# Kernel optimization log

Hardware: AMD Instinct MI355X
Metric: run time of the kernel (lower is better)

## Reference

```python
import jax, jax.numpy as jnp
import numpy as np

N = 50000      # nodes
E = 800000     # edges (avg degree 16)
IN = 256       # in_features
F1 = 32        # gnn_features per head
F2 = 32        # out_features per head
H = 8          # heads
NEG_SLOPE = 0.2


def setup_inputs() -> dict:
    key = jax.random.key(0)
    ks = jax.random.split(key, 12)
    s = 0.05
    return {
        "x":   jax.random.normal(ks[0], (N, IN), jnp.float32),
        "W1":  jax.random.normal(ks[1], (IN, H * F1), jnp.float32) * s,
        "al1": jax.random.normal(ks[2], (H, F1), jnp.float32) * s,
        "ar1": jax.random.normal(ks[3], (H, F1), jnp.float32) * s,
        "b1":  jnp.zeros((H, F1), jnp.float32),
        "W2":  jax.random.normal(ks[4], (F1, H * F2), jnp.float32) * s,
        "al2": jax.random.normal(ks[5], (H, F2), jnp.float32) * s,
        "ar2": jax.random.normal(ks[6], (H, F2), jnp.float32) * s,
        "b2":  jnp.zeros((H, F2), jnp.float32),
        "src": jax.random.randint(ks[7], (E,), 0, N, jnp.int32),
        "dst": jax.random.randint(ks[8], (E,), 0, N, jnp.int32),
    }


def _gat_layer(x, W, al, ar, b, src, dst):
    """One DGL-style GATConv. x:[N,Fin] -> [N,H,F]."""
    n, h, f = x.shape[0], al.shape[0], al.shape[1]
    z = (x @ W).reshape(n, h, f)                      # [N,H,F] projected feats
    el = jnp.einsum('nhf,hf->nh', z, al)              # src attention logits
    er = jnp.einsum('nhf,hf->nh', z, ar)              # dst attention logits
    e = el[src] + er[dst]                             # [E,H]
    e = jnp.where(e >= 0, e, NEG_SLOPE * e)           # LeakyReLU(0.2)
    # segmented (per-destination) softmax over incoming edges
    m = jax.ops.segment_max(e, dst, num_segments=n)   # [N,H]
    ex = jnp.exp(e - m[dst])                          # [E,H]
    denom = jax.ops.segment_sum(ex, dst, num_segments=n)
    alpha = ex / denom[dst]                           # [E,H]
    # weighted scatter-aggregate
    out = jax.ops.segment_sum(alpha[:, :, None] * z[src], dst, num_segments=n)
    return out + b[None]                              # [N,H,F]


def reference(x, W1, al1, ar1, b1, W2, al2, ar2, b2, src, dst):
    h = _gat_layer(x, W1, al1, ar1, b1, src, dst).mean(axis=1)   # [N,F1]
    h = jax.nn.elu(h)                                            # Dropout(0.5) = identity in eval
    out = _gat_layer(h, W2, al2, ar2, b2, src, dst).mean(axis=1) # [N,F2]
    return out
```

## Files before the change

### kernel.cpp

```cpp
#include <hip/hip_runtime.h>
#include <hip/hip_fp16.h>
#include <math.h>

#define IN_F 256
#define NHEAD 8
#define FDIM 32
#define SCAN_B 512

__device__ inline unsigned pkh2(float x, float y) {
  __half2 h = __floats2half2_rn(x, y);
  return *reinterpret_cast<unsigned*>(&h);
}


__global__ __launch_bounds__(256) void hist_k(const int* __restrict__ dst,
                                              int* __restrict__ deg, int E) {
  int i = blockIdx.x * 256 + threadIdx.x;
  if (i < E) atomicAdd(&deg[dst[i]], 1);
}

__global__ __launch_bounds__(SCAN_B) void scan1_k(const int* __restrict__ deg,
                                                  int* __restrict__ offs,
                                                  int* __restrict__ bsum, int N) {
  __shared__ int s[SCAN_B];
  int t = threadIdx.x;
  int i = blockIdx.x * SCAN_B + t;
  s[t] = (i < N) ? deg[i] : 0;
  __syncthreads();
  for (int off = 1; off < SCAN_B; off <<= 1) {
    int add = (t >= off) ? s[t - off] : 0;
    __syncthreads();
    s[t] += add;
    __syncthreads();
  }
  if (i < N) offs[i + 1] = s[t];
  if (t == SCAN_B - 1) bsum[blockIdx.x] = s[t];
}

__global__ __launch_bounds__(SCAN_B) void scan2_k(int* __restrict__ bsum, int nb) {
  __shared__ int s[SCAN_B];
  int t = threadIdx.x;
  s[t] = (t < nb) ? bsum[t] : 0;
  __syncthreads();
  for (int off = 1; off < SCAN_B; off <<= 1) {
    int add = (t >= off) ? s[t - off] : 0;
    __syncthreads();
    s[t] += add;
    __syncthreads();
  }
  if (t < nb) bsum[t] = (t == 0) ? 0 : s[t - 1];
}

__global__ __launch_bounds__(SCAN_B) void scan3_k(int* __restrict__ offs,
                                                  const int* __restrict__ bsum, int N) {
  int i = blockIdx.x * SCAN_B + threadIdx.x;
  if (i < N) offs[i + 1] += bsum[blockIdx.x];
  if (i == 0) offs[0] = 0;
}

__global__ __launch_bounds__(256) void scatter_k(const int* __restrict__ src,
                                                 const int* __restrict__ dst,
                                                 const int* __restrict__ offs,
                                                 int* __restrict__ cursor,
                                                 int* __restrict__ esrc, int E) {
  int i = blockIdx.x * 256 + threadIdx.x;
  if (i < E) {
    int d = dst[i];
    int pos = offs[d] + atomicAdd(&cursor[d], 1);
    esrc[pos] = src[i];
  }
}

__global__ __launch_bounds__(256) void gemm_xw_k(const float* __restrict__ A,
                                                 const float* __restrict__ B,
                                                 __half* __restrict__ Zh, int M) {
  __shared__ float AsF[16 * 196];
  __shared__ float BsF[16 * 196];
  int t = threadIdx.x;
  int tx = t & 15, ty = t >> 4;
  int row0 = blockIdx.x * 128, col0 = blockIdx.y * 128;
  float acc[8][8] = {};
  for (int kt = 0; kt < 256; kt += 16) {
#pragma unroll
    for (int i = 0; i < 2; ++i) {
      int idx = t + i * 256;
      int row = idx >> 2, q = idx & 3;
      float4 va = make_float4(0.f, 0.f, 0.f, 0.f);
      if (row0 + row < M)
        va = *reinterpret_cast<const float4*>(&A[(size_t)(row0 + row) * 256 + kt + q * 4]);
      int abase = (row >> 3) * 12 + (row & 7);
      AsF[(q * 4 + 0) * 196 + abase] = va.x;
      AsF[(q * 4 + 1) * 196 + abase] = va.y;
      AsF[(q * 4 + 2) * 196 + abase] = va.z;
      AsF[(q * 4 + 3) * 196 + abase] = va.w;
      int brow = idx >> 5, bc = idx & 31;
      float4 vb = *reinterpret_cast<const float4*>(&B[(size_t)(kt + brow) * 256 + col0 + bc * 4]);
      *reinterpret_cast<float4*>(&BsF[brow * 196 + (bc >> 1) * 12 + (bc & 1) * 4]) = vb;
    }
    __syncthreads();
#pragma unroll
    for (int kk = 0; kk < 16; ++kk) {
      float a[8], b[8];
      *reinterpret_cast<float4*>(&a[0]) = *reinterpret_cast<const float4*>(&AsF[kk * 196 + ty * 12]);
      *reinterpret_cast<float4*>(&a[4]) = *reinterpret_cast<const float4*>(&AsF[kk * 196 + ty * 12 + 4]);
      *reinterpret_cast<float4*>(&b[0]) = *reinterpret_cast<const float4*>(&BsF[kk * 196 + tx * 12]);
      *reinterpret_cast<float4*>(&b[4]) = *reinterpret_cast<const float4*>(&BsF[kk * 196 + tx * 12 + 4]);
#pragma unroll
      for (int i = 0; i < 8; ++i)
#pragma unroll
        for (int j = 0; j < 8; ++j) acc[i][j] = fmaf(a[i], b[j], acc[i][j]);
    }
    __syncthreads();
  }
#pragma unroll
  for (int i = 0; i < 8; ++i) {
    int r = row0 + ty * 8 + i;
    if (r < M) {
      uint4 w;
      w.x = pkh2(acc[i][0], acc[i][1]);
      w.y = pkh2(acc[i][2], acc[i][3]);
      w.z = pkh2(acc[i][4], acc[i][5]);
      w.w = pkh2(acc[i][6], acc[i][7]);
      *reinterpret_cast<uint4*>(&Zh[(size_t)r * 256 + col0 + tx * 8]) = w;
    }
  }
}

__global__ __launch_bounds__(256) void gemm_h_k(const float* __restrict__ Hmat,
                                                const float* __restrict__ W2,
                                                __half* __restrict__ Zh, int M) {
  __shared__ float Ws[32][256];
  __shared__ float Hs[32][20];
  int t = threadIdx.x;
  for (int i = t; i < 32 * 256; i += 256) Ws[i >> 8][i & 255] = W2[i];
  int row0 = blockIdx.x * 16;
  for (int i = t; i < 16 * 32; i += 256) {
    int r = i >> 5, k = i & 31;
    Hs[k][r] = (row0 + r < M) ? Hmat[(size_t)(row0 + r) * 32 + k] : 0.f;
  }
  __syncthreads();
  int tx = t & 63, ty = t >> 6;
  float acc[4][4] = {};
#pragma unroll
  for (int k = 0; k < 32; ++k) {
    float4 a4 = *reinterpret_cast<const float4*>(&Hs[k][ty * 4]);
    float4 b4 = *reinterpret_cast<const float4*>(&Ws[k][tx * 4]);
    float a[4] = {a4.x, a4.y, a4.z, a4.w};
    float b[4] = {b4.x, b4.y, b4.z, b4.w};
#pragma unroll
    for (int i = 0; i < 4; ++i)
#pragma unroll
      for (int j = 0; j < 4; ++j) acc[i][j] = fmaf(a[i], b[j], acc[i][j]);
  }
#pragma unroll
  for (int i = 0; i < 4; ++i) {
    int r = row0 + ty * 4 + i;
    if (r < M) {
      uint2 w;
      w.x = pkh2(acc[i][0], acc[i][1]);
      w.y = pkh2(acc[i][2], acc[i][3]);
      *reinterpret_cast<uint2*>(&Zh[(size_t)r * 256 + tx * 4]) = w;
    }
  }
}

__global__ __launch_bounds__(256) void logits_k(const __half* __restrict__ Zh,
                                                const float* __restrict__ al,
                                                const float* __restrict__ ar,
                                                float* __restrict__ el,
                                                float* __restrict__ er, int N) {
  int wave = threadIdx.x >> 6;
  int lane = threadIdx.x & 63;
  int n = blockIdx.x * 4 + wave;
  if (n >= N) return;
  uint2 u = *reinterpret_cast<const uint2*>(&Zh[(size_t)n * 256 + lane * 4]);
  float2 f0 = __half22float2(*reinterpret_cast<__half2*>(&u.x));
  float2 f1 = __half22float2(*reinterpret_cast<__half2*>(&u.y));
  float4 a4 = reinterpret_cast<const float4*>(al)[lane];
  float4 r4 = reinterpret_cast<const float4*>(ar)[lane];
  float pl = f0.x * a4.x + f0.y * a4.y + f1.x * a4.z + f1.y * a4.w;
  float pr = f0.x * r4.x + f0.y * r4.y + f1.x * r4.z + f1.y * r4.w;
  pl += __shfl_xor(pl, 1); pl += __shfl_xor(pl, 2); pl += __shfl_xor(pl, 4);
  pr += __shfl_xor(pr, 1); pr += __shfl_xor(pr, 2); pr += __shfl_xor(pr, 4);
  if ((lane & 7) == 0) {
    int h = lane >> 3;
    el[(size_t)n * 8 + h] = pl;
    er[(size_t)n * 8 + h] = pr;
  }
}

__global__ __launch_bounds__(256) void alpha_k(const float* __restrict__ el,
                                               const float* __restrict__ er,
                                               const int* __restrict__ offs,
                                               const int* __restrict__ esrc,
                                               float* __restrict__ alf,
                                               float* __restrict__ rden, int N) {
  int g = blockIdx.x * 256 + threadIdx.x;
  if (g >= N * NHEAD) return;
  int n = g >> 3, h = g & 7;
  int beg = offs[n], end = offs[n + 1];
  float er_h = er[g];
  float m = -INFINITY;
  for (int i = beg; i < end; ++i) {
    float e = el[(size_t)esrc[i] * 8 + h] + er_h;
    e = (e >= 0.f) ? e : 0.2f * e;
    m = fmaxf(m, e);
  }
  float s = 0.f;
  for (int i = beg; i < end; ++i) {
    float e = el[(size_t)esrc[i] * 8 + h] + er_h;
    e = (e >= 0.f) ? e : 0.2f * e;
    float ex = __expf(e - m);
    alf[(size_t)i * 8 + h] = ex;
    s += ex;
  }
  rden[g] = (end > beg) ? 1.f / s : 0.f;
}

template <bool LAYER1>
__global__ __launch_bounds__(256) void agg_k(const __half* __restrict__ Zh,
                                             const float* __restrict__ alf,
                                             const float* __restrict__ rden,
                                             const float* __restrict__ bias,
                                             const int* __restrict__ offs,
                                             const int* __restrict__ esrc,
                                             float* __restrict__ out, int N) {
  int wid = threadIdx.x >> 6, lane = threadIdx.x & 63;
  int n = blockIdx.x * 4 + wid;
  if (n >= N) return;
  int h = lane >> 3, q = lane & 7;
  int beg = offs[n], end = offs[n + 1];
  float4 acc = make_float4(0.f, 0.f, 0.f, 0.f);
#pragma unroll 4
  for (int i = beg; i < end; ++i) {
    int sidx = esrc[i];
    float a = alf[(size_t)i * 8 + h];
    uint2 u = *reinterpret_cast<const uint2*>(&Zh[(size_t)sidx * 256 + h * 32 + q * 4]);
    float2 f0 = __half22float2(*reinterpret_cast<__half2*>(&u.x));
    float2 f1 = __half22float2(*reinterpret_cast<__half2*>(&u.y));
    acc.x = fmaf(a, f0.x, acc.x);
    acc.y = fmaf(a, f0.y, acc.y);
    acc.z = fmaf(a, f1.x, acc.z);
    acc.w = fmaf(a, f1.y, acc.w);
  }
  float r = rden[(size_t)n * 8 + h];
  float4 b4 = *reinterpret_cast<const float4*>(&bias[h * 32 + q * 4]);
  float4 v;
  v.x = fmaf(acc.x, r, b4.x);
  v.y = fmaf(acc.y, r, b4.y);
  v.z = fmaf(acc.z, r, b4.z);
  v.w = fmaf(acc.w, r, b4.w);
#pragma unroll
  for (int off = 8; off < 64; off <<= 1) {
    v.x += __shfl_xor(v.x, off);
    v.y += __shfl_xor(v.y, off);
    v.z += __shfl_xor(v.z, off);
    v.w += __shfl_xor(v.w, off);
  }
  if (h == 0) {
    v.x *= 0.125f; v.y *= 0.125f; v.z *= 0.125f; v.w *= 0.125f;
    if (LAYER1) {
      v.x = (v.x > 0.f) ? v.x : expm1f(v.x);
      v.y = (v.y > 0.f) ? v.y : expm1f(v.y);
      v.z = (v.z > 0.f) ? v.z : expm1f(v.z);
      v.w = (v.w > 0.f) ? v.w : expm1f(v.w);
    }
    *reinterpret_cast<float4*>(&out[(size_t)n * 32 + q * 4]) = v;
  }
}


extern "C" void kernel_launch(void* const* d_in, const int* in_sizes, int n_in,
                              void* d_out, int out_size, void* d_ws, size_t ws_size,
                              hipStream_t stream) {
  const float* x   = (const float*)d_in[0];
  const float* W1  = (const float*)d_in[1];
  const float* al1 = (const float*)d_in[2];
  const float* ar1 = (const float*)d_in[3];
  const float* b1  = (const float*)d_in[4];
  const float* W2  = (const float*)d_in[5];
  const float* al2 = (const float*)d_in[6];
  const float* ar2 = (const float*)d_in[7];
  const float* b2  = (const float*)d_in[8];
  const int* src   = (const int*)d_in[9];
  const int* dst   = (const int*)d_in[10];
  float* out = (float*)d_out;

  const int N = in_sizes[0] / IN_F;
  const int E = in_sizes[9];

  char* p = (char*)d_ws;
  auto alloc = [&](size_t bytes) {
    char* q = p;
    p += (bytes + 255) & ~(size_t)255;
    return q;
  };
  __half* zh  = (__half*)alloc((size_t)N * 256 * 2);
  float* el   = (float*)alloc((size_t)N * 8 * 4);
  float* er   = (float*)alloc((size_t)N * 8 * 4);
  float* h1   = (float*)alloc((size_t)N * 32 * 4);
  float* alf  = (float*)alloc((size_t)E * 8 * 4);
  float* rden = (float*)alloc((size_t)N * 8 * 4);
  int* offs   = (int*)alloc((size_t)(N + 1) * 4);
  int* deg    = (int*)alloc((size_t)N * 4);
  int* cursor = (int*)alloc((size_t)N * 4);
  int* bsum   = (int*)alloc((size_t)SCAN_B * 4);
  int* esrc   = (int*)alloc((size_t)E * 4);

  hipMemsetAsync(deg, 0, (size_t)N * 4, stream);
  hipMemsetAsync(cursor, 0, (size_t)N * 4, stream);

  int nb = (N + SCAN_B - 1) / SCAN_B;
  hist_k<<<(E + 255) / 256, 256, 0, stream>>>(dst, deg, E);
  scan1_k<<<nb, SCAN_B, 0, stream>>>(deg, offs, bsum, N);
  scan2_k<<<1, SCAN_B, 0, stream>>>(bsum, nb);
  scan3_k<<<nb, SCAN_B, 0, stream>>>(offs, bsum, N);
  scatter_k<<<(E + 255) / 256, 256, 0, stream>>>(src, dst, offs, cursor, esrc, E);

  int nh_blocks = (N * NHEAD + 255) / 256;

  dim3 g1((N + 127) / 128, 2);
  gemm_xw_k<<<g1, 256, 0, stream>>>(x, W1, zh, N);
  logits_k<<<(N + 3) / 4, 256, 0, stream>>>(zh, al1, ar1, el, er, N);
  alpha_k<<<nh_blocks, 256, 0, stream>>>(el, er, offs, esrc, alf, rden, N);
  agg_k<true><<<(N + 3) / 4, 256, 0, stream>>>(zh, alf, rden, b1, offs, esrc, h1, N);

  gemm_h_k<<<(N + 15) / 16, 256, 0, stream>>>(h1, W2, zh, N);
  logits_k<<<(N + 3) / 4, 256, 0, stream>>>(zh, al2, ar2, el, er, N);
  alpha_k<<<nh_blocks, 256, 0, stream>>>(el, er, offs, esrc, alf, rden, N);
  agg_k<false><<<(N + 3) / 4, 256, 0, stream>>>(zh, alf, rden, b2, offs, esrc, out, N);
}
```

Before: 513.5 us.

## Replace FP32 SIMT projection GEMM with FP16 MFMA kernel using pre-transposed W1

The first-layer projection x@W1 now runs on MFMA 16x16x32 f16 instructions instead of a shared-memory tiled FP32 FMA GEMM. A small new kernel converts W1 to half and transposes it. The GEMM keeps each wave's A fragment in registers, converted from fp32 on load, and streams B straight from global memory (L2-resident) with no LDS staging. The trade-off is lower-precision inputs (fp16 x and W1), scalar 2-byte output stores, and one extra kernel launch.

After: 483.0 us. 6.0% less time.

```diff
diff --git a/kernel.cpp b/kernel.cpp
--- a/kernel.cpp
+++ b/kernel.cpp
@@ -6,6 +6,9 @@
 #define NHEAD 8
 #define FDIM 32
 #define SCAN_B 512
+
+typedef _Float16 f16x8 __attribute__((ext_vector_type(8)));
+typedef float f32x4 __attribute__((ext_vector_type(4)));
 
 __device__ inline unsigned pkh2(float x, float y) {
   __half2 h = __floats2half2_rn(x, y);
@@ -71,57 +74,55 @@
   }
 }
 
-__global__ __launch_bounds__(256) void gemm_xw_k(const float* __restrict__ A,
-                                                 const float* __restrict__ B,
-                                                 __half* __restrict__ Zh, int M) {
-  __shared__ float AsF[16 * 196];
-  __shared__ float BsF[16 * 196];
+__global__ __launch_bounds__(256) void w1cvt_k(const float* __restrict__ W1,
+                                               __half* __restrict__ W1t) {
+  __shared__ float s[16][17];
+  int bx = blockIdx.x * 16, by = blockIdx.y * 16;
+  int tx = threadIdx.x, ty = threadIdx.y;
+  s[ty][tx] = W1[(by + ty) * 256 + bx + tx];
+  __syncthreads();
+  W1t[(size_t)(bx + ty) * 256 + by + tx] = __float2half(s[tx][ty]);
+}
+
+__global__ __launch_bounds__(256) void gemm_xw_mfma_k(const float* __restrict__ X,
+                                                      const __half* __restrict__ W1t,
+                                                      __half* __restrict__ Zh, int M) {
   int t = threadIdx.x;
-  int tx = t & 15, ty = t >> 4;
-  int row0 = blockIdx.x * 128, col0 = blockIdx.y * 128;
-  float acc[8][8] = {};
-  for (int kt = 0; kt < 256; kt += 16) {
-#pragma unroll
-    for (int i = 0; i < 2; ++i) {
-      int idx = t + i * 256;
-      int row = idx >> 2, q = idx & 3;
-      float4 va = make_float4(0.f, 0.f, 0.f, 0.f);
-      if (row0 + row < M)
-        va = *reinterpret_cast<const float4*>(&A[(size_t)(row0 + row) * 256 + kt + q * 4]);
-      int abase = (row >> 3) * 12 + (row & 7);
-      AsF[(q * 4 + 0) * 196 + abase] = va.x;
-      AsF[(q * 4 + 1) * 196 + abase] = va.y;
-      AsF[(q * 4 + 2) * 196 + abase] = va.z;
-      AsF[(q * 4 + 3) * 196 + abase] = va.w;
-      int brow = idx >> 5, bc = idx & 31;
-      float4 vb = *reinterpret_cast<const float4*>(&B[(size_t)(kt + brow) * 256 + col0 + bc * 4]);
-      *reinterpret_cast<float4*>(&BsF[brow * 196 + (bc >> 1) * 12 + (bc & 1) * 4]) = vb;
+  int wv = t >> 6, l = t & 63;
+  int r = l & 15, kg = l >> 4;
+  int row0 = blockIdx.x * 64 + wv * 16;
+  int row = row0 + r;
+  int rowc = (row < M) ? row : (M - 1);
+
+  f16x8 a[8];
+  const float* xp = X + (size_t)rowc * 256 + kg * 8;
+#pragma unroll
+  for (int ks = 0; ks < 8; ++ks) {
+    float4 f0 = *reinterpret_cast<const float4*>(xp + ks * 32);
+    float4 f1 = *reinterpret_cast<const float4*>(xp + ks * 32 + 4);
+    f16x8 av;
+    av[0] = (_Float16)f0.x; av[1] = (_Float16)f0.y;
+    av[2] = (_Float16)f0.z; av[3] = (_Float16)f0.w;
+    av[4] = (_Float16)f1.x; av[5] = (_Float16)f1.y;
+    av[6] = (_Float16)f1.z; av[7] = (_Float16)f1.w;
+    a[ks] = av;
+  }
+
+#pragma unroll 4
+  for (int nf = 0; nf < 16; ++nf) {
+    int col = nf * 16 + r;
+    const f16x8* bp = reinterpret_cast<const f16x8*>(W1t + (size_t)col * 256 + kg * 8);
+    f32x4 acc = {0.f, 0.f, 0.f, 0.f};
+#pragma unroll
+    for (int ks = 0; ks < 8; ++ks) {
+      f16x8 bv = bp[ks * 4];
+      acc = __builtin_amdgcn_mfma_f32_16x16x32_f16(a[ks], bv, acc, 0, 0, 0);
     }
-    __syncthreads();
-#pragma unroll
-    for (int kk = 0; kk < 16; ++kk) {
-      float a[8], b[8];
-      *reinterpret_cast<float4*>(&a[0]) = *reinterpret_cast<const float4*>(&AsF[kk * 196 + ty * 12]);
-      *reinterpret_cast<float4*>(&a[4]) = *reinterpret_cast<const float4*>(&AsF[kk * 196 + ty * 12 + 4]);
-      *reinterpret_cast<float4*>(&b[0]) = *reinterpret_cast<const float4*>(&BsF[kk * 196 + tx * 12]);
-      *reinterpret_cast<float4*>(&b[4]) = *reinterpret_cast<const float4*>(&BsF[kk * 196 + tx * 12 + 4]);
-#pragma unroll
-      for (int i = 0; i < 8; ++i)
-#pragma unroll
-        for (int j = 0; j < 8; ++j) acc[i][j] = fmaf(a[i], b[j], acc[i][j]);
-    }
-    __syncthreads();
-  }
-#pragma unroll
-  for (int i = 0; i < 8; ++i) {
-    int r = row0 + ty * 8 + i;
-    if (r < M) {
-      uint4 w;
-      w.x = pkh2(acc[i][0], acc[i][1]);
-      w.y = pkh2(acc[i][2], acc[i][3]);
-      w.z = pkh2(acc[i][4], acc[i][5]);
-      w.w = pkh2(acc[i][6], acc[i][7]);
-      *reinterpret_cast<uint4*>(&Zh[(size_t)r * 256 + col0 + tx * 8]) = w;
+    int orow = row0 + kg * 4;
+#pragma unroll
+    for (int i = 0; i < 4; ++i) {
+      if (orow + i < M)
+        Zh[(size_t)(orow + i) * 256 + nf * 16 + r] = __float2half((float)acc[i]);
     }
   }
 }
@@ -296,6 +297,7 @@
     return q;
   };
   __half* zh  = (__half*)alloc((size_t)N * 256 * 2);
+  __half* w1t = (__half*)alloc((size_t)256 * 256 * 2);
   float* el   = (float*)alloc((size_t)N * 8 * 4);
   float* er   = (float*)alloc((size_t)N * 8 * 4);
   float* h1   = (float*)alloc((size_t)N * 32 * 4);
@@ -319,8 +321,8 @@
 
   int nh_blocks = (N * NHEAD + 255) / 256;
 
-  dim3 g1((N + 127) / 128, 2);
-  gemm_xw_k<<<g1, 256, 0, stream>>>(x, W1, zh, N);
+  w1cvt_k<<<dim3(16, 16), dim3(16, 16), 0, stream>>>(W1, w1t);
+  gemm_xw_mfma_k<<<(N + 63) / 64, 256, 0, stream>>>(x, w1t, zh, N);
   logits_k<<<(N + 3) / 4, 256, 0, stream>>>(zh, al1, ar1, el, er, N);
   alpha_k<<<nh_blocks, 256, 0, stream>>>(el, er, offs, esrc, alf, rden, N);
   agg_k<true><<<(N + 3) / 4, 256, 0, stream>>>(zh, alf, rden, b1, offs, esrc, h1, N);
```
